# Kernel optimization log

Measured on AMD Instinct MI355X. Metric: run time of the kernel, lower is better.

Reference implementation:

```python
import jax, jax.numpy as jnp
import numpy as np

B, T, LQ, LC = 8, 256, 20, 10
DIM, H = 128, 8
VDIM, WDIM, CDIM = 1024, 300, 50
WORDS, CHARS = 10000, 100


def _build_edges(T, B):
    """Replicates build_graph_edges(hops=2) + build_semantic_edges + build_query_edges,
    then expand_edge_index_for_batch with num_nodes = T + 1.  Static numpy (jit-safe)."""
    N = T + 1
    es = []
    for h in (1, 2):  # temporal edges, 2 hops (indices replicate original code exactly)
        i = np.arange(T - h)
        es += [np.stack([i, i + h]), np.stack([i + h, i])]
    i = np.arange(T)  # query<->segment edges inside build_graph_edges
    z = np.zeros(T, dtype=np.int64)
    es += [np.stack([z, i + 1]), np.stack([i + 1, z])]
    temporal = np.concatenate(es, axis=1)
    a, b = np.triu_indices(T, k=1)  # torch.combinations(arange(T), r=2)
    sem = np.concatenate([np.stack([a, b]), np.stack([b, a])], axis=1)
    qe = np.stack([np.concatenate([[0], np.arange(1, T + 1)]),
                   np.concatenate([np.arange(1, T + 1), [0]])])
    off = (np.arange(B, dtype=np.int64) * N)[None, :, None]
    expand = lambda e: (e[:, None, :].astype(np.int64) + off).reshape(2, -1)
    return np.concatenate([expand(temporal), expand(sem), expand(qe)], axis=1)


def setup_inputs() -> dict:
    key = jax.random.key(0)
    ks = jax.random.split(key, 16)
    w = lambda k, shape: jax.random.normal(k, shape, jnp.float32) * 0.02
    return {
        "word_ids": jax.random.randint(ks[0], (B, LQ), 0, WORDS),
        "char_ids": jax.random.randint(ks[1], (B, LQ, LC), 0, CHARS),
        "video_features": jax.random.normal(ks[2], (B, T, VDIM), jnp.float32),
        "v_mask": jnp.ones((B, T), jnp.float32),
        "q_mask": jnp.ones((B, LQ), jnp.float32),
        "word_emb": w(ks[3], (WORDS, WDIM)),
        "char_emb": w(ks[4], (CHARS, CDIM)),
        "W_embed": w(ks[5], (WDIM + CDIM, DIM)), "b_embed": jnp.zeros((DIM,), jnp.float32),
        "W_vproj": w(ks[6], (VDIM, DIM)), "b_vproj": jnp.zeros((DIM,), jnp.float32),
        "W_enc": w(ks[7], (DIM, DIM)), "b_enc": jnp.zeros((DIM,), jnp.float32),
        "Wq": w(ks[8], (DIM, DIM)), "bq": jnp.zeros((DIM,), jnp.float32),
        "Wk": w(ks[9], (DIM, DIM)), "bk": jnp.zeros((DIM,), jnp.float32),
        "Wv": w(ks[10], (DIM, DIM)), "bv": jnp.zeros((DIM,), jnp.float32),
        "Wskip": w(ks[11], (DIM, DIM)), "bskip": jnp.zeros((DIM,), jnp.float32),
        "W_start": w(ks[12], (DIM, 1)), "b_start": jnp.zeros((1,), jnp.float32),
        "W_end": w(ks[13], (DIM, 1)), "b_end": jnp.zeros((1,), jnp.float32),
    }


def reference(word_ids, char_ids, video_features, v_mask, q_mask,
              word_emb, char_emb, W_embed, b_embed, W_vproj, b_vproj,
              W_enc, b_enc, Wq, bq, Wk, bk, Wv, bv, Wskip, bskip,
              W_start, b_start, W_end, b_end):
    enc = lambda x, m: jax.nn.relu(x @ W_enc + b_enc) * m[..., None]  # shared feature encoder (stand-in)
    # video branch
    vfeat = enc(video_features @ W_vproj + b_vproj, v_mask)            # [B, T, DIM]
    # query branch: word + char embeddings -> dim, encode, mean-pool
    qemb = jnp.concatenate([word_emb[word_ids], char_emb[char_ids].mean(axis=2)], axis=-1)
    qfeat = enc(qemb @ W_embed + b_embed, q_mask).mean(axis=1)         # [B, DIM]
    nodes = jnp.concatenate([qfeat[:, None, :], vfeat], axis=1)        # [B, N, DIM], N = T+1
    Bn, N, _ = nodes.shape
    Nn = Bn * N
    xf = nodes.reshape(Nn, DIM)
    edges = jnp.asarray(_build_edges(N - 1, Bn))                       # [2, E] static
    src, dst = edges[0], edges[1]                                      # PyG: messages x_j=src -> target i=dst
    hd = DIM // H
    q = (xf @ Wq + bq).reshape(Nn, H, hd)
    k = (xf @ Wk + bk).reshape(Nn, H, hd)
    v = (xf @ Wv + bv).reshape(Nn, H, hd)
    # TransformerConv: per-edge attention logits, segment-softmax over incoming edges
    logits = (q[dst] * k[src]).sum(-1) / float(np.sqrt(hd))            # [E, H]
    mx = jax.ops.segment_max(logits, dst, num_segments=Nn)
    ex = jnp.exp(logits - mx[dst])
    den = jax.ops.segment_sum(ex, dst, num_segments=Nn)
    alpha = ex / (den[dst] + 1e-16)
    agg = jax.ops.segment_sum(alpha[:, :, None] * v[src], dst, num_segments=Nn)  # [Nn, H, hd]
    out = agg.reshape(Nn, DIM) + xf @ Wskip + bskip                    # root_weight skip connection
    out = out.reshape(Bn, N, DIM)
    start_logits = (out[:, 1:] @ W_start + b_start)[..., 0]            # [B, T]
    end_logits = (out[:, 1:] @ W_end + b_end)[..., 0]                  # [B, T]
    return start_logits, end_logits
```

## Files before the change

### kernel.cpp

```cpp
#include <hip/hip_runtime.h>
#include <hip/hip_bf16.h>
#include <math.h>

#define B_ 8
#define T_ 256
#define LQ_ 20
#define LC_ 10
#define DIM_ 128
#define N_ 257
#define NN_ (B_*N_)

#define FMA4(a, s, ww) { (a).x += (s)*(ww).x; (a).y += (s)*(ww).y; (a).z += (s)*(ww).z; (a).w += (s)*(ww).w; }

__global__ __launch_bounds__(512) void kNODE(
    const float* __restrict__ video, const float* __restrict__ Wv,
    const float* __restrict__ bvp,
    const float* __restrict__ We, const float* __restrict__ be,
    const float* __restrict__ vmask,
    const int* __restrict__ word_ids, const int* __restrict__ char_ids,
    const float* __restrict__ word_emb, const float* __restrict__ char_emb,
    const float* __restrict__ W_embed, const float* __restrict__ b_embed,
    const float* __restrict__ q_mask,
    const float* __restrict__ Wq, const float* __restrict__ bq,
    const float* __restrict__ Wk, const float* __restrict__ bk,
    const float* __restrict__ Wvv, const float* __restrict__ bval,
    const float* __restrict__ Ws, const float* __restrict__ bs,
    float* __restrict__ q, float* __restrict__ k,
    float* __restrict__ v, float* __restrict__ sk,
    float* __restrict__ eq)
{
  __shared__ __align__(16) float smem_f[19008];
  float4* ps4 = reinterpret_cast<float4*>(smem_f);
  float* hl = smem_f + 16896;
  float* xe = smem_f + 17952;
  const int blk = blockIdx.x, tid = threadIdx.x;
  const float* Wm[4] = {Wq, Wk, Wvv, Ws};
  const float* bm[4] = {bq, bk, bval, bs};
  float* om[4] = {q, k, v, sk};

  if (blk < 256) {
    const int r0 = blk * 8;
    {
      const float4* src = reinterpret_cast<const float4*>(video + (size_t)r0 * 1024);
      #pragma unroll
      for (int i = 0; i < 4; ++i) {
        const int idx4 = tid + i * 512;
        const int r = idx4 >> 8, f = idx4 & 255;
        *reinterpret_cast<float4*>(&smem_f[r * 1028 + f * 4]) = src[r * 256 + f];
      }
    }
    __syncthreads();
    const int c4 = tid & 31, ks = tid >> 5;
    float4 acc[8];
    #pragma unroll
    for (int r = 0; r < 8; ++r) acc[r] = float4{0.f, 0.f, 0.f, 0.f};
    {
      const float4* W4 = reinterpret_cast<const float4*>(Wv) + c4;
      for (int kc = 0; kc < 16; ++kc) {
        const int k0 = ks * 64 + kc * 4;
        const float4 w0 = W4[(size_t)(k0 + 0) * 32];
        const float4 w1 = W4[(size_t)(k0 + 1) * 32];
        const float4 w2 = W4[(size_t)(k0 + 2) * 32];
        const float4 w3 = W4[(size_t)(k0 + 3) * 32];
        #pragma unroll
        for (int r = 0; r < 8; ++r) {
          const float4 rv = *reinterpret_cast<const float4*>(&smem_f[r * 1028 + k0]);
          FMA4(acc[r], rv.x, w0); FMA4(acc[r], rv.y, w1);
          FMA4(acc[r], rv.z, w2); FMA4(acc[r], rv.w, w3);
        }
      }
    }
    __syncthreads();
    #pragma unroll
    for (int r = 0; r < 8; ++r) ps4[(ks * 8 + r) * 33 + c4] = acc[r];
    __syncthreads();
    if (tid < 256) {
      const int r = tid >> 5, c = tid & 31;
      float4 s = reinterpret_cast<const float4*>(bvp)[c];
      #pragma unroll
      for (int ke = 0; ke < 16; ++ke) {
        const float4 p = ps4[(ke * 8 + r) * 33 + c];
        s.x += p.x; s.y += p.y; s.z += p.z; s.w += p.w;
      }
      *reinterpret_cast<float4*>(&hl[r * 132 + c * 4]) = s;
    }
    __syncthreads();
    #pragma unroll
    for (int r = 0; r < 8; ++r) acc[r] = float4{0.f, 0.f, 0.f, 0.f};
    {
      const float4* We4 = reinterpret_cast<const float4*>(We) + c4;
      #pragma unroll
      for (int kc = 0; kc < 2; ++kc) {
        const int k0 = ks * 8 + kc * 4;
        const float4 w0 = We4[(size_t)(k0 + 0) * 32];
        const float4 w1 = We4[(size_t)(k0 + 1) * 32];
        const float4 w2 = We4[(size_t)(k0 + 2) * 32];
        const float4 w3 = We4[(size_t)(k0 + 3) * 32];
        #pragma unroll
        for (int r = 0; r < 8; ++r) {
          const float4 rv = *reinterpret_cast<const float4*>(&hl[r * 132 + k0]);
          FMA4(acc[r], rv.x, w0); FMA4(acc[r], rv.y, w1);
          FMA4(acc[r], rv.z, w2); FMA4(acc[r], rv.w, w3);
        }
      }
    }
    #pragma unroll
    for (int r = 0; r < 8; ++r) ps4[(ks * 8 + r) * 33 + c4] = acc[r];
    __syncthreads();
    if (tid < 256) {
      const int r = tid >> 5, c = tid & 31;
      float4 s = reinterpret_cast<const float4*>(be)[c];
      #pragma unroll
      for (int ke = 0; ke < 16; ++ke) {
        const float4 p = ps4[(ke * 8 + r) * 33 + c];
        s.x += p.x; s.y += p.y; s.z += p.z; s.w += p.w;
      }
      const float mk = vmask[r0 + r];
      s.x = fmaxf(s.x, 0.f) * mk; s.y = fmaxf(s.y, 0.f) * mk;
      s.z = fmaxf(s.z, 0.f) * mk; s.w = fmaxf(s.w, 0.f) * mk;
      *reinterpret_cast<float4*>(&xe[r * 132 + c * 4]) = s;
    }
    __syncthreads();
    const int m = ks >> 2, keP = ks & 3;
    #pragma unroll
    for (int r = 0; r < 8; ++r) acc[r] = float4{0.f, 0.f, 0.f, 0.f};
    {
      const float4* Wp4 = reinterpret_cast<const float4*>(Wm[m]) + c4;
      #pragma unroll
      for (int kc = 0; kc < 8; ++kc) {
        const int k0 = keP * 32 + kc * 4;
        const float4 w0 = Wp4[(size_t)(k0 + 0) * 32];
        const float4 w1 = Wp4[(size_t)(k0 + 1) * 32];
        const float4 w2 = Wp4[(size_t)(k0 + 2) * 32];
        const float4 w3 = Wp4[(size_t)(k0 + 3) * 32];
        #pragma unroll
        for (int r = 0; r < 8; ++r) {
          const float4 rv = *reinterpret_cast<const float4*>(&xe[r * 132 + k0]);
          FMA4(acc[r], rv.x, w0); FMA4(acc[r], rv.y, w1);
          FMA4(acc[r], rv.z, w2); FMA4(acc[r], rv.w, w3);
        }
      }
    }
    #pragma unroll
    for (int r = 0; r < 8; ++r) ps4[(ks * 8 + r) * 33 + c4] = acc[r];
    __syncthreads();
    #pragma unroll
    for (int it = 0; it < 2; ++it) {
      const int id = tid + it * 512;
      const int mm = id >> 8, r = (id >> 5) & 7, c = id & 31;
      float4 s = reinterpret_cast<const float4*>(bm[mm])[c];
      #pragma unroll
      for (int ke = 0; ke < 4; ++ke) {
        const float4 p = ps4[((mm * 4 + ke) * 8 + r) * 33 + c];
        s.x += p.x; s.y += p.y; s.z += p.z; s.w += p.w;
      }
      const int vr = r0 + r;
      const int node = (vr >> 8) * 257 + 1 + (vr & 255);
      *reinterpret_cast<float4*>(om[mm] + (size_t)node * 128 + 4 * c) = s;
    }
  } else {
    const int qi = blk - 256;
    const int b = qi / 20, lq = qi - b * 20;
    float* emb = smem_f;
    float* ps  = emb + 352;
    float* hq  = emb + 608;
    float* pe  = emb + 736;
    const int wid = word_ids[b * LQ_ + lq];
    for (int m2 = tid; m2 < 300; m2 += 512) emb[m2] = word_emb[(size_t)wid * 300 + m2];
    if (tid < 50) {
      float s = 0.f;
      #pragma unroll
      for (int l = 0; l < 10; ++l) {
        const int cid = char_ids[(b * LQ_ + lq) * 10 + l];
        s += char_emb[cid * 50 + tid];
      }
      emb[300 + tid] = s * 0.1f;
    }
    __syncthreads();
    const int j = tid & 127, half = tid >> 7;
    if (tid < 256) {
      float a = 0.f;
      const float* Wcol = W_embed + (size_t)(half * 175) * 128 + j;
      const float* eh = emb + half * 175;
      #pragma unroll 5
      for (int m2 = 0; m2 < 175; ++m2) a += eh[m2] * Wcol[(size_t)m2 * 128];
      ps[half * 128 + j] = a;
    }
    __syncthreads();
    if (tid < 128) hq[tid] = ps[tid] + ps[128 + tid] + b_embed[tid];
    __syncthreads();
    if (tid < 256) {
      float e = 0.f;
      #pragma unroll 8
      for (int kk = 0; kk < 64; ++kk)
        e += hq[half * 64 + kk] * We[(half * 64 + kk) * 128 + j];
      pe[half * 128 + j] = e;
    }
    __syncthreads();
    if (tid < 128) {
      float ev = pe[tid] + pe[128 + tid] + be[tid];
      ev = fmaxf(ev, 0.f) * q_mask[b * LQ_ + lq];
      eq[(size_t)qi * 128 + tid] = ev;
    }
  }
}

__device__ __forceinline__ float cntf(int dnode, int s) {
  if (dnode == 256) return (s == 0 ? 1.f : 0.f) + (s == 255 ? 1.f : 0.f);
  float c = (s != dnode) ? 1.f : 0.f;
  if (s == 0) c += 1.f;
  if (s == dnode - 1) c += 2.f;
  if (s == dnode + 1 && dnode <= 254) c += 1.f;
  if (s == dnode - 2 && dnode >= 2) c += 1.f;
  if (s == dnode + 2 && dnode <= 253) c += 1.f;
  return c;
}

__global__ __launch_bounds__(256) void kATTN(
    const float* __restrict__ q, const float* __restrict__ k,
    const float* __restrict__ v, const float* __restrict__ eq,
    const float* __restrict__ Wk, const float* __restrict__ bk,
    const float* __restrict__ Wvv, const float* __restrict__ bval,
    float* __restrict__ npart, float* __restrict__ dpart)
{
  __shared__ float Kl[32][128];
  __shared__ float Vl[32][128];
  __shared__ float m0[128];
  const int d0 = blockIdx.x * 32;
  const int y  = blockIdx.y;
  const int b  = blockIdx.z;
  const int tid = threadIdx.x;
  const int base = b * 257;
  const int s0 = y * 32;
  {
    const float4* ksrc = reinterpret_cast<const float4*>(k + (size_t)(base + s0) * 128);
    const float4* vsrc = reinterpret_cast<const float4*>(v + (size_t)(base + s0) * 128);
    float4* kd = reinterpret_cast<float4*>(Kl);
    float4* vd = reinterpret_cast<float4*>(Vl);
    #pragma unroll
    for (int i = 0; i < 4; ++i) {
      kd[tid + i * 256] = ksrc[tid + i * 256];
      vd[tid + i * 256] = vsrc[tid + i * 256];
    }
  }
  if (y == 0 && tid < 128) {
    float s = 0.f;
    #pragma unroll 4
    for (int lq = 0; lq < LQ_; ++lq) s += eq[((size_t)b * LQ_ + lq) * 128 + tid];
    m0[tid] = s * (1.f / LQ_);
  }
  const int dd = tid >> 3, h = tid & 7;
  const int dnode = d0 + dd + 1;
  const float* qrow = q + (size_t)(base + dnode) * 128 + h * 16;
  const float4 qq0 = *(const float4*)(qrow + 0);
  const float4 qq1 = *(const float4*)(qrow + 4);
  const float4 qq2 = *(const float4*)(qrow + 8);
  const float4 qq3 = *(const float4*)(qrow + 12);
  __syncthreads();
  if (y == 0) {
    const int j = tid & 127, half = tid >> 7;
    const float* W = half ? Wvv : Wk;
    float acc = half ? bval[j] : bk[j];
    #pragma unroll 8
    for (int kk = 0; kk < 128; ++kk) acc += m0[kk] * W[kk * 128 + j];
    if (half) Vl[0][j] = acc; else Kl[0][j] = acc;
  }
  __syncthreads();

  float den = 0.f;
  float4 o0 = {0,0,0,0}, o1 = {0,0,0,0}, o2 = {0,0,0,0}, o3 = {0,0,0,0};
  #pragma unroll 2
  for (int s = 0; s < 32; ++s) {
    const float* krow = &Kl[s][h * 16];
    const float4 k0 = *(const float4*)(krow + 0);
    const float4 k1 = *(const float4*)(krow + 4);
    const float4 k2 = *(const float4*)(krow + 8);
    const float4 k3 = *(const float4*)(krow + 12);
    float dt = qq0.x*k0.x + qq0.y*k0.y + qq0.z*k0.z + qq0.w*k0.w
             + qq1.x*k1.x + qq1.y*k1.y + qq1.z*k1.z + qq1.w*k1.w
             + qq2.x*k2.x + qq2.y*k2.y + qq2.z*k2.z + qq2.w*k2.w
             + qq3.x*k3.x + qq3.y*k3.y + qq3.z*k3.z + qq3.w*k3.w;
    const float c = cntf(dnode, s0 + s);
    const float pw = c * __expf(dt * 0.25f);
    den += pw;
    const float* vrow = &Vl[s][h * 16];
    const float4 v0 = *(const float4*)(vrow + 0);
    const float4 v1 = *(const float4*)(vrow + 4);
    const float4 v2 = *(const float4*)(vrow + 8);
    const float4 v3 = *(const float4*)(vrow + 12);
    o0.x += pw*v0.x; o0.y += pw*v0.y; o0.z += pw*v0.z; o0.w += pw*v0.w;
    o1.x += pw*v1.x; o1.y += pw*v1.y; o1.z += pw*v1.z; o1.w += pw*v1.w;
    o2.x += pw*v2.x; o2.y += pw*v2.y; o2.z += pw*v2.z; o2.w += pw*v2.w;
    o3.x += pw*v3.x; o3.y += pw*v3.y; o3.z += pw*v3.z; o3.w += pw*v3.w;
  }
  const size_t pb = ((size_t)y * 8 + b) * 256 + d0;
  float* np = npart + (pb + dd) * 128 + h * 16;
  *reinterpret_cast<float4*>(np + 0)  = o0;
  *reinterpret_cast<float4*>(np + 4)  = o1;
  *reinterpret_cast<float4*>(np + 8)  = o2;
  *reinterpret_cast<float4*>(np + 12) = o3;
  dpart[(pb + dd) * 8 + h] = den;
}

__global__ __launch_bounds__(256) void kRED(
    const float* __restrict__ npart, const float* __restrict__ dpart,
    const float* __restrict__ sk,
    const float* __restrict__ W_start, const float* __restrict__ b_start,
    const float* __restrict__ W_end, const float* __restrict__ b_end,
    float* __restrict__ out)
{
  __shared__ float red[16][2][2];
  const int d0 = blockIdx.x * 16;
  const int b = blockIdx.y;
  const int tid = threadIdx.x;
  const int base = b * 257;
  const int jB = tid & 127, shB = tid >> 7;
  const int hB = jB >> 4;
  const float wst = W_start[jB], wen = W_end[jB];
  #pragma unroll
  for (int dd8 = 0; dd8 < 8; ++dd8) {
    const int dd = shB * 8 + dd8;
    const int dst = d0 + dd;
    float num = 0.f, den = 0.f;
    #pragma unroll
    for (int y = 0; y < 8; ++y) {
      const size_t pb = ((size_t)y * 8 + b) * 256 + dst;
      num += npart[pb * 128 + jB];
      den += dpart[pb * 8 + hB];
    }
    const float o = num / (den + 1e-16f) + sk[(size_t)(base + dst + 1) * 128 + jB];
    float psum = o * wst, pesum = o * wen;
    #pragma unroll
    for (int off = 1; off < 64; off <<= 1) {
      psum += __shfl_xor(psum, off);
      pesum += __shfl_xor(pesum, off);
    }
    if ((tid & 63) == 0) { red[dd][jB >> 6][0] = psum; red[dd][jB >> 6][1] = pesum; }
  }
  __syncthreads();
  if (tid < 16) {
    out[b * 256 + d0 + tid]        = red[tid][0][0] + red[tid][1][0] + b_start[0];
    out[2048 + b * 256 + d0 + tid] = red[tid][0][1] + red[tid][1][1] + b_end[0];
  }
}

extern "C" void kernel_launch(void* const* d_in, const int* in_sizes, int n_in,
                              void* d_out, int out_size, void* d_ws, size_t ws_size,
                              hipStream_t stream) {
  const int*   word_ids = (const int*)d_in[0];
  const int*   char_ids = (const int*)d_in[1];
  const float* video    = (const float*)d_in[2];
  const float* v_mask   = (const float*)d_in[3];
  const float* q_mask   = (const float*)d_in[4];
  const float* word_emb = (const float*)d_in[5];
  const float* char_emb = (const float*)d_in[6];
  const float* W_embed  = (const float*)d_in[7];
  const float* b_embed  = (const float*)d_in[8];
  const float* W_vproj  = (const float*)d_in[9];
  const float* b_vproj  = (const float*)d_in[10];
  const float* W_enc    = (const float*)d_in[11];
  const float* b_enc    = (const float*)d_in[12];
  const float* Wq       = (const float*)d_in[13];
  const float* bq       = (const float*)d_in[14];
  const float* Wk       = (const float*)d_in[15];
  const float* bk       = (const float*)d_in[16];
  const float* Wv       = (const float*)d_in[17];
  const float* bv       = (const float*)d_in[18];
  const float* Wskip    = (const float*)d_in[19];
  const float* bskip    = (const float*)d_in[20];
  const float* W_start  = (const float*)d_in[21];
  const float* b_start  = (const float*)d_in[22];
  const float* W_end    = (const float*)d_in[23];
  const float* b_end    = (const float*)d_in[24];

  float* q     = (float*)d_ws;
  float* k     = q  + NN_ * DIM_;
  float* v     = k  + NN_ * DIM_;
  float* sk    = v  + NN_ * DIM_;
  float* eq    = sk + NN_ * DIM_;
  float* npart = eq + 160 * 128;
  float* dpart = npart + (size_t)8 * 8 * 256 * 128;

  hipLaunchKernelGGL(kNODE, dim3(416), dim3(512), 0, stream,
    video, W_vproj, b_vproj, W_enc, b_enc, v_mask,
    word_ids, char_ids, word_emb, char_emb, W_embed, b_embed, q_mask,
    Wq, bq, Wk, bk, Wv, bv, Wskip, bskip, q, k, v, sk, eq);
  hipLaunchKernelGGL(kATTN, dim3(8, 8, 8), dim3(256), 0, stream,
    q, k, v, eq, Wk, bk, Wv, bv, npart, dpart);
  hipLaunchKernelGGL(kRED, dim3(16, 8), dim3(256), 0, stream,
    npart, dpart, sk, W_start, b_start, W_end, b_end, (float*)d_out);
}
```

Measured before the change: 60.48 us.

## Move video projection GEMM onto bf16 MFMA with split-precision hi/lo operands

The 2048x1024x128 video projection now runs in its own kernel using bf16 MFMA instructions instead of fp32 FMA loops. Each fp32 operand is split into high and low bf16 parts, and three MFMA products are summed to keep accuracy close to fp32. A pre-kernel converts W_vproj to transposed hi/lo bf16 every call and also computes the query embeddings. The K dimension is split across two blocks whose partial sums are added in the follow-on kernel. The goal is to replace the slow fp32 FMA GEMM with matrix-core throughput, at the cost of two extra launches, extra global round trips for the partials and converted weights, and small precision differences.

```diff
diff --git a/kernel.cpp b/kernel.cpp
--- a/kernel.cpp
+++ b/kernel.cpp
@@ -12,22 +12,169 @@
 
 #define FMA4(a, s, ww) { (a).x += (s)*(ww).x; (a).y += (s)*(ww).y; (a).z += (s)*(ww).z; (a).w += (s)*(ww).w; }
 
-__global__ __launch_bounds__(512) void kNODE(
-    const float* __restrict__ video, const float* __restrict__ Wv,
-    const float* __restrict__ bvp,
-    const float* __restrict__ We, const float* __restrict__ be,
-    const float* __restrict__ vmask,
+typedef __attribute__((ext_vector_type(8))) short bf16x8;
+typedef __attribute__((ext_vector_type(4))) float f32x4;
+
+__device__ __forceinline__ unsigned short f2bf(float f) {
+  unsigned u = __float_as_uint(f);
+  unsigned r = u + 0x7FFFu + ((u >> 16) & 1u);
+  return (unsigned short)(r >> 16);
+}
+__device__ __forceinline__ float bf2f(unsigned short h) {
+  return __uint_as_float(((unsigned)h) << 16);
+}
+
+__global__ __launch_bounds__(256) void kPRE(
     const int* __restrict__ word_ids, const int* __restrict__ char_ids,
     const float* __restrict__ word_emb, const float* __restrict__ char_emb,
     const float* __restrict__ W_embed, const float* __restrict__ b_embed,
+    const float* __restrict__ We, const float* __restrict__ be,
     const float* __restrict__ q_mask,
+    const float* __restrict__ Wv,
+    float* __restrict__ eq,
+    unsigned short* __restrict__ WvTh, unsigned short* __restrict__ WvTl)
+{
+  __shared__ __align__(16) float smem[2112];
+  const int blk = blockIdx.x, tid = threadIdx.x;
+  if (blk < 160) {
+    const int qi = blk;
+    const int b = qi / 20, lq = qi - b * 20;
+    float* emb = smem;
+    float* ps  = emb + 352;
+    float* hq  = emb + 608;
+    float* pe  = emb + 736;
+    const int wid = word_ids[b * LQ_ + lq];
+    for (int m2 = tid; m2 < 300; m2 += 256) emb[m2] = word_emb[(size_t)wid * 300 + m2];
+    if (tid < 50) {
+      float s = 0.f;
+      #pragma unroll
+      for (int l = 0; l < 10; ++l) {
+        const int cid = char_ids[(b * LQ_ + lq) * 10 + l];
+        s += char_emb[cid * 50 + tid];
+      }
+      emb[300 + tid] = s * 0.1f;
+    }
+    __syncthreads();
+    const int j = tid & 127, half = tid >> 7;
+    {
+      float a = 0.f;
+      const float* Wcol = W_embed + (size_t)(half * 175) * 128 + j;
+      const float* eh = emb + half * 175;
+      #pragma unroll 5
+      for (int m2 = 0; m2 < 175; ++m2) a += eh[m2] * Wcol[(size_t)m2 * 128];
+      ps[half * 128 + j] = a;
+    }
+    __syncthreads();
+    if (tid < 128) hq[tid] = ps[tid] + ps[128 + tid] + b_embed[tid];
+    __syncthreads();
+    {
+      float e = 0.f;
+      #pragma unroll 8
+      for (int kk = 0; kk < 64; ++kk)
+        e += hq[half * 64 + kk] * We[(half * 64 + kk) * 128 + j];
+      pe[half * 128 + j] = e;
+    }
+    __syncthreads();
+    if (tid < 128) {
+      float ev = pe[tid] + pe[128 + tid] + be[tid];
+      ev = fmaxf(ev, 0.f) * q_mask[b * LQ_ + lq];
+      eq[(size_t)qi * 128 + tid] = ev;
+    }
+  } else {
+    const int k0 = (blk - 160) * 16;
+    const float4* src = reinterpret_cast<const float4*>(Wv + (size_t)k0 * 128);
+    #pragma unroll
+    for (int i = 0; i < 2; ++i) {
+      const int idx4 = tid + i * 256;
+      const int r = idx4 >> 5, f = idx4 & 31;
+      *reinterpret_cast<float4*>(&smem[r * 132 + f * 4]) = src[r * 32 + f];
+    }
+    __syncthreads();
+    const int col = tid & 127, kg = tid >> 7;
+    bf16x8 vh, vl;
+    #pragma unroll
+    for (int j = 0; j < 8; ++j) {
+      const int kk = kg * 8 + j;
+      const float xv = smem[kk * 132 + col];
+      const unsigned short hi = f2bf(xv);
+      const unsigned short lo = f2bf(xv - bf2f(hi));
+      vh[j] = (short)hi; vl[j] = (short)lo;
+    }
+    *reinterpret_cast<bf16x8*>(WvTh + (size_t)col * 1024 + k0 + kg * 8) = vh;
+    *reinterpret_cast<bf16x8*>(WvTl + (size_t)col * 1024 + k0 + kg * 8) = vl;
+  }
+}
+
+__global__ __launch_bounds__(512) void kVID(
+    const float* __restrict__ video,
+    const unsigned short* __restrict__ WvTh,
+    const unsigned short* __restrict__ WvTl,
+    float* __restrict__ h2)
+{
+  __shared__ unsigned short Ah[16 * 512];
+  __shared__ unsigned short Al[16 * 512];
+  const int blk = blockIdx.x, tid = threadIdx.x;
+  const int rt = blk >> 1, kh = blk & 1;
+  const int r0 = rt * 16;
+  #pragma unroll
+  for (int i = 0; i < 2; ++i) {
+    const int g = tid * 2 + i;
+    const int row = g >> 6, gk = g & 63;
+    const float* src = video + (size_t)(r0 + row) * 1024 + kh * 512 + gk * 8;
+    const float4 x0 = *reinterpret_cast<const float4*>(src);
+    const float4 x1 = *reinterpret_cast<const float4*>(src + 4);
+    const float xs[8] = {x0.x, x0.y, x0.z, x0.w, x1.x, x1.y, x1.z, x1.w};
+    bf16x8 vh, vl;
+    #pragma unroll
+    for (int j = 0; j < 8; ++j) {
+      const unsigned short hi = f2bf(xs[j]);
+      const unsigned short lo = f2bf(xs[j] - bf2f(hi));
+      vh[j] = (short)hi; vl[j] = (short)lo;
+    }
+    int byteoff = row * 1024 + gk * 16;
+    byteoff ^= ((row & 7) << 4);
+    *reinterpret_cast<bf16x8*>(reinterpret_cast<char*>(Ah) + byteoff) = vh;
+    *reinterpret_cast<bf16x8*>(reinterpret_cast<char*>(Al) + byteoff) = vl;
+  }
+  __syncthreads();
+  const int wv = tid >> 6, lane = tid & 63;
+  const int col16 = lane & 15, kg8 = lane >> 4;
+  const int c0 = wv * 16;
+  const unsigned short* pBh = WvTh + (size_t)(c0 + col16) * 1024 + kh * 512;
+  const unsigned short* pBl = WvTl + (size_t)(c0 + col16) * 1024 + kh * 512;
+  const int arow = lane & 15;
+  const int abase = arow * 1024;
+  f32x4 acc = {0.f, 0.f, 0.f, 0.f};
+  #pragma unroll 4
+  for (int t = 0; t < 16; ++t) {
+    const int kb = t * 32 + kg8 * 8;
+    const int aoff = (abase + kb * 2) ^ ((arow & 7) << 4);
+    const bf16x8 ah = *reinterpret_cast<const bf16x8*>(reinterpret_cast<const char*>(Ah) + aoff);
+    const bf16x8 al = *reinterpret_cast<const bf16x8*>(reinterpret_cast<const char*>(Al) + aoff);
+    const bf16x8 bh = *reinterpret_cast<const bf16x8*>(pBh + kb);
+    const bf16x8 bl = *reinterpret_cast<const bf16x8*>(pBl + kb);
+    acc = __builtin_amdgcn_mfma_f32_16x16x32_bf16(ah, bh, acc, 0, 0, 0);
+    acc = __builtin_amdgcn_mfma_f32_16x16x32_bf16(ah, bl, acc, 0, 0, 0);
+    acc = __builtin_amdgcn_mfma_f32_16x16x32_bf16(al, bh, acc, 0, 0, 0);
+  }
+  const int ocol = c0 + col16;
+  const int orow = (lane >> 4) * 4;
+  float* hdst = h2 + (size_t)kh * 2048 * 128;
+  #pragma unroll
+  for (int i2 = 0; i2 < 4; ++i2)
+    hdst[(size_t)(r0 + orow + i2) * 128 + ocol] = acc[i2];
+}
+
+__global__ __launch_bounds__(512) void kMAIN(
+    const float* __restrict__ h2, const float* __restrict__ bvp,
+    const float* __restrict__ We, const float* __restrict__ be,
+    const float* __restrict__ vmask,
     const float* __restrict__ Wq, const float* __restrict__ bq,
     const float* __restrict__ Wk, const float* __restrict__ bk,
     const float* __restrict__ Wvv, const float* __restrict__ bval,
     const float* __restrict__ Ws, const float* __restrict__ bs,
     float* __restrict__ q, float* __restrict__ k,
-    float* __restrict__ v, float* __restrict__ sk,
-    float* __restrict__ eq)
+    float* __restrict__ v, float* __restrict__ sk)
 {
   __shared__ __align__(16) float smem_f[19008];
   float4* ps4 = reinterpret_cast<float4*>(smem_f);
@@ -37,171 +184,91 @@
   const float* Wm[4] = {Wq, Wk, Wvv, Ws};
   const float* bm[4] = {bq, bk, bval, bs};
   float* om[4] = {q, k, v, sk};
-
-  if (blk < 256) {
-    const int r0 = blk * 8;
-    {
-      const float4* src = reinterpret_cast<const float4*>(video + (size_t)r0 * 1024);
+  const int r0 = blk * 8;
+  if (tid < 256) {
+    const int r = tid >> 5, c = tid & 31;
+    const float4 p0 = *reinterpret_cast<const float4*>(h2 + (size_t)(r0 + r) * 128 + c * 4);
+    const float4 p1 = *reinterpret_cast<const float4*>(h2 + (size_t)(2048 + r0 + r) * 128 + c * 4);
+    float4 s = reinterpret_cast<const float4*>(bvp)[c];
+    s.x += p0.x + p1.x; s.y += p0.y + p1.y;
+    s.z += p0.z + p1.z; s.w += p0.w + p1.w;
+    *reinterpret_cast<float4*>(&hl[r * 132 + c * 4]) = s;
+  }
+  __syncthreads();
+  const int c4 = tid & 31, ks = tid >> 5;
+  float4 acc[8];
+  #pragma unroll
+  for (int r = 0; r < 8; ++r) acc[r] = float4{0.f, 0.f, 0.f, 0.f};
+  {
+    const float4* We4 = reinterpret_cast<const float4*>(We) + c4;
+    #pragma unroll
+    for (int kc = 0; kc < 2; ++kc) {
+      const int k0 = ks * 8 + kc * 4;
+      const float4 w0 = We4[(size_t)(k0 + 0) * 32];
+      const float4 w1 = We4[(size_t)(k0 + 1) * 32];
+      const float4 w2 = We4[(size_t)(k0 + 2) * 32];
+      const float4 w3 = We4[(size_t)(k0 + 3) * 32];
       #pragma unroll
-      for (int i = 0; i < 4; ++i) {
-        const int idx4 = tid + i * 512;
-        const int r = idx4 >> 8, f = idx4 & 255;
-        *reinterpret_cast<float4*>(&smem_f[r * 1028 + f * 4]) = src[r * 256 + f];
+      for (int r = 0; r < 8; ++r) {
+        const float4 rv = *reinterpret_cast<const float4*>(&hl[r * 132 + k0]);
+        FMA4(acc[r], rv.x, w0); FMA4(acc[r], rv.y, w1);
+        FMA4(acc[r], rv.z, w2); FMA4(acc[r], rv.w, w3);
       }
     }
-    __syncthreads();
-    const int c4 = tid & 31, ks = tid >> 5;
-    float4 acc[8];
-    #pragma unroll
-    for (int r = 0; r < 8; ++r) acc[r] = float4{0.f, 0.f, 0.f, 0.f};
-    {
-      const float4* W4 = reinterpret_cast<const float4*>(Wv) + c4;
-      for (int kc = 0; kc < 16; ++kc) {
-        const int k0 = ks * 64 + kc * 4;
-        const float4 w0 = W4[(size_t)(k0 + 0) * 32];
-        const float4 w1 = W4[(size_t)(k0 + 1) * 32];
-        const float4 w2 = W4[(size_t)(k0 + 2) * 32];
-        const float4 w3 = W4[(size_t)(k0 + 3) * 32];
-        #pragma unroll
-        for (int r = 0; r < 8; ++r) {
-          const float4 rv = *reinterpret_cast<const float4*>(&smem_f[r * 1028 + k0]);
-          FMA4(acc[r], rv.x, w0); FMA4(acc[r], rv.y, w1);
-          FMA4(acc[r], rv.z, w2); FMA4(acc[r], rv.w, w3);
-        }
+  }
+  #pragma unroll
+  for (int r = 0; r < 8; ++r) ps4[(ks * 8 + r) * 33 + c4] = acc[r];
+  __syncthreads();
+  if (tid < 256) {
+    const int r = tid >> 5, c = tid & 31;
+    float4 s = reinterpret_cast<const float4*>(be)[c];
+    #pragma unroll
+    for (int ke = 0; ke < 16; ++ke) {
+      const float4 p = ps4[(ke * 8 + r) * 33 + c];
+      s.x += p.x; s.y += p.y; s.z += p.z; s.w += p.w;
+    }
+    const float mk = vmask[r0 + r];
+    s.x = fmaxf(s.x, 0.f) * mk; s.y = fmaxf(s.y, 0.f) * mk;
+    s.z = fmaxf(s.z, 0.f) * mk; s.w = fmaxf(s.w, 0.f) * mk;
+    *reinterpret_cast<float4*>(&xe[r * 132 + c * 4]) = s;
+  }
+  __syncthreads();
+  const int m = ks >> 2, keP = ks & 3;
+  #pragma unroll
+  for (int r = 0; r < 8; ++r) acc[r] = float4{0.f, 0.f, 0.f, 0.f};
+  {
+    const float4* Wp4 = reinterpret_cast<const float4*>(Wm[m]) + c4;
+    #pragma unroll
+    for (int kc = 0; kc < 8; ++kc) {
+      const int k0 = keP * 32 + kc * 4;
+      const float4 w0 = Wp4[(size_t)(k0 + 0) * 32];
+      const float4 w1 = Wp4[(size_t)(k0 + 1) * 32];
+      const float4 w2 = Wp4[(size_t)(k0 + 2) * 32];
+      const float4 w3 = Wp4[(size_t)(k0 + 3) * 32];
+      #pragma unroll
+      for (int r = 0; r < 8; ++r) {
+        const float4 rv = *reinterpret_cast<const float4*>(&xe[r * 132 + k0]);
+        FMA4(acc[r], rv.x, w0); FMA4(acc[r], rv.y, w1);
+        FMA4(acc[r], rv.z, w2); FMA4(acc[r], rv.w, w3);
       }
     }
-    __syncthreads();
-    #pragma unroll
-    for (int r = 0; r < 8; ++r) ps4[(ks * 8 + r) * 33 + c4] = acc[r];
-    __syncthreads();
-    if (tid < 256) {
-      const int r = tid >> 5, c = tid & 31;
-      float4 s = reinterpret_cast<const float4*>(bvp)[c];
-      #pragma unroll
-      for (int ke = 0; ke < 16; ++ke) {
-        const float4 p = ps4[(ke * 8 + r) * 33 + c];
-        s.x += p.x; s.y += p.y; s.z += p.z; s.w += p.w;
-      }
-      *reinterpret_cast<float4*>(&hl[r * 132 + c * 4]) = s;
-    }
-    __syncthreads();
-    #pragma unroll
-    for (int r = 0; r < 8; ++r) acc[r] = float4{0.f, 0.f, 0.f, 0.f};
-    {
-      const float4* We4 = reinterpret_cast<const float4*>(We) + c4;
-      #pragma unroll
-      for (int kc = 0; kc < 2; ++kc) {
-        const int k0 = ks * 8 + kc * 4;
-        const float4 w0 = We4[(size_t)(k0 + 0) * 32];
-        const float4 w1 = We4[(size_t)(k0 + 1) * 32];
-        const float4 w2 = We4[(size_t)(k0 + 2) * 32];
-        const float4 w3 = We4[(size_t)(k0 + 3) * 32];
-        #pragma unroll
-        for (int r = 0; r < 8; ++r) {
-          const float4 rv = *reinterpret_cast<const float4*>(&hl[r * 132 + k0]);
-          FMA4(acc[r], rv.x, w0); FMA4(acc[r], rv.y, w1);
-          FMA4(acc[r], rv.z, w2); FMA4(acc[r], rv.w, w3);
-        }
-      }
-    }
-    #pragma unroll
-    for (int r = 0; r < 8; ++r) ps4[(ks * 8 + r) * 33 + c4] = acc[r];
-    __syncthreads();
-    if (tid < 256) {
-      const int r = tid >> 5, c = tid & 31;
-      float4 s = reinterpret_cast<const float4*>(be)[c];
-      #pragma unroll
-      for (int ke = 0; ke < 16; ++ke) {
-        const float4 p = ps4[(ke * 8 + r) * 33 + c];
-        s.x += p.x; s.y += p.y; s.z += p.z; s.w += p.w;
-      }
-      const float mk = vmask[r0 + r];
-      s.x = fmaxf(s.x, 0.f) * mk; s.y = fmaxf(s.y, 0.f) * mk;
-      s.z = fmaxf(s.z, 0.f) * mk; s.w = fmaxf(s.w, 0.f) * mk;
-      *reinterpret_cast<float4*>(&xe[r * 132 + c * 4]) = s;
-    }
-    __syncthreads();
-    const int m = ks >> 2, keP = ks & 3;
-    #pragma unroll
-    for (int r = 0; r < 8; ++r) acc[r] = float4{0.f, 0.f, 0.f, 0.f};
-    {
-      const float4* Wp4 = reinterpret_cast<const float4*>(Wm[m]) + c4;
-      #pragma unroll
-      for (int kc = 0; kc < 8; ++kc) {
-        const int k0 = keP * 32 + kc * 4;
-        const float4 w0 = Wp4[(size_t)(k0 + 0) * 32];
-        const float4 w1 = Wp4[(size_t)(k0 + 1) * 32];
-        const float4 w2 = Wp4[(size_t)(k0 + 2) * 32];
-        const float4 w3 = Wp4[(size_t)(k0 + 3) * 32];
-        #pragma unroll
-        for (int r = 0; r < 8; ++r) {
-          const float4 rv = *reinterpret_cast<const float4*>(&xe[r * 132 + k0]);
-          FMA4(acc[r], rv.x, w0); FMA4(acc[r], rv.y, w1);
-          FMA4(acc[r], rv.z, w2); FMA4(acc[r], rv.w, w3);
-        }
-      }
-    }
-    #pragma unroll
-    for (int r = 0; r < 8; ++r) ps4[(ks * 8 + r) * 33 + c4] = acc[r];
-    __syncthreads();
-    #pragma unroll
-    for (int it = 0; it < 2; ++it) {
-      const int id = tid + it * 512;
-      const int mm = id >> 8, r = (id >> 5) & 7, c = id & 31;
-      float4 s = reinterpret_cast<const float4*>(bm[mm])[c];
-      #pragma unroll
-      for (int ke = 0; ke < 4; ++ke) {
-        const float4 p = ps4[((mm * 4 + ke) * 8 + r) * 33 + c];
-        s.x += p.x; s.y += p.y; s.z += p.z; s.w += p.w;
-      }
-      const int vr = r0 + r;
-      const int node = (vr >> 8) * 257 + 1 + (vr & 255);
-      *reinterpret_cast<float4*>(om[mm] + (size_t)node * 128 + 4 * c) = s;
-    }
-  } else {
-    const int qi = blk - 256;
-    const int b = qi / 20, lq = qi - b * 20;
-    float* emb = smem_f;
-    float* ps  = emb + 352;
-    float* hq  = emb + 608;
-    float* pe  = emb + 736;
-    const int wid = word_ids[b * LQ_ + lq];
-    for (int m2 = tid; m2 < 300; m2 += 512) emb[m2] = word_emb[(size_t)wid * 300 + m2];
-    if (tid < 50) {
-      float s = 0.f;
-      #pragma unroll
-      for (int l = 0; l < 10; ++l) {
-        const int cid = char_ids[(b * LQ_ + lq) * 10 + l];
-        s += char_emb[cid * 50 + tid];
-      }
-      emb[300 + tid] = s * 0.1f;
-    }
-    __syncthreads();
-    const int j = tid & 127, half = tid >> 7;
-    if (tid < 256) {
-      float a = 0.f;
-      const float* Wcol = W_embed + (size_t)(half * 175) * 128 + j;
-      const float* eh = emb + half * 175;
-      #pragma unroll 5
-      for (int m2 = 0; m2 < 175; ++m2) a += eh[m2] * Wcol[(size_t)m2 * 128];
-      ps[half * 128 + j] = a;
-    }
-    __syncthreads();
-    if (tid < 128) hq[tid] = ps[tid] + ps[128 + tid] + b_embed[tid];
-    __syncthreads();
-    if (tid < 256) {
-      float e = 0.f;
-      #pragma unroll 8
-      for (int kk = 0; kk < 64; ++kk)
-        e += hq[half * 64 + kk] * We[(half * 64 + kk) * 128 + j];
-      pe[half * 128 + j] = e;
-    }
-    __syncthreads();
-    if (tid < 128) {
-      float ev = pe[tid] + pe[128 + tid] + be[tid];
-      ev = fmaxf(ev, 0.f) * q_mask[b * LQ_ + lq];
-      eq[(size_t)qi * 128 + tid] = ev;
-    }
+  }
+  #pragma unroll
+  for (int r = 0; r < 8; ++r) ps4[(ks * 8 + r) * 33 + c4] = acc[r];
+  __syncthreads();
+  #pragma unroll
+  for (int it = 0; it < 2; ++it) {
+    const int id = tid + it * 512;
+    const int mm = id >> 8, r = (id >> 5) & 7, c = id & 31;
+    float4 s = reinterpret_cast<const float4*>(bm[mm])[c];
+    #pragma unroll
+    for (int ke = 0; ke < 4; ++ke) {
+      const float4 p = ps4[((mm * 4 + ke) * 8 + r) * 33 + c];
+      s.x += p.x; s.y += p.y; s.z += p.z; s.w += p.w;
+    }
+    const int vr = r0 + r;
+    const int node = (vr >> 8) * 257 + 1 + (vr & 255);
+    *reinterpret_cast<float4*>(om[mm] + (size_t)node * 128 + 4 * c) = s;
   }
 }
 
@@ -380,11 +447,18 @@
   float* eq    = sk + NN_ * DIM_;
   float* npart = eq + 160 * 128;
   float* dpart = npart + (size_t)8 * 8 * 256 * 128;
-
-  hipLaunchKernelGGL(kNODE, dim3(416), dim3(512), 0, stream,
-    video, W_vproj, b_vproj, W_enc, b_enc, v_mask,
-    word_ids, char_ids, word_emb, char_emb, W_embed, b_embed, q_mask,
-    Wq, bq, Wk, bk, Wv, bv, Wskip, bskip, q, k, v, sk, eq);
+  float* h2    = dpart + 16384;
+  unsigned short* WvTh = (unsigned short*)(h2 + (size_t)2 * 2048 * 128);
+  unsigned short* WvTl = WvTh + 128 * 1024;
+
+  hipLaunchKernelGGL(kPRE, dim3(224), dim3(256), 0, stream,
+    word_ids, char_ids, word_emb, char_emb, W_embed, b_embed,
+    W_enc, b_enc, q_mask, W_vproj, eq, WvTh, WvTl);
+  hipLaunchKernelGGL(kVID, dim3(256), dim3(512), 0, stream,
+    video, WvTh, WvTl, h2);
+  hipLaunchKernelGGL(kMAIN, dim3(256), dim3(512), 0, stream,
+    h2, b_vproj, W_enc, b_enc, v_mask,
+    Wq, bq, Wk, bk, Wv, bv, Wskip, bskip, q, k, v, sk);
   hipLaunchKernelGGL(kATTN, dim3(8, 8, 8), dim3(256), 0, stream,
     q, k, v, eq, Wk, bk, Wv, bv, npart, dpart);
   hipLaunchKernelGGL(kRED, dim3(16, 8), dim3(256), 0, stream,
```

After: 65.49 us. 8.3% more time.

## Project V onto start/end heads before attention to shrink partial outputs

Applied to the files above, without the earlier changes.

Because the start and end heads are linear, each V row is pre-multiplied by the W_start and W_end head slices inside the attention kernel. Each query then accumulates two scalars per head instead of a 16-wide vector. This cuts the partial-numerator buffer from 128 floats per node per split to 2 per head, and removes most of the reduction kernel's global reads. The cost is an extra small shared-memory projection and sync per block, plus a change in floating-point summation order.

```diff
diff --git a/kernel.cpp b/kernel.cpp
--- a/kernel.cpp
+++ b/kernel.cpp
@@ -221,11 +221,15 @@
     const float* __restrict__ v, const float* __restrict__ eq,
     const float* __restrict__ Wk, const float* __restrict__ bk,
     const float* __restrict__ Wvv, const float* __restrict__ bval,
-    float* __restrict__ npart, float* __restrict__ dpart)
+    const float* __restrict__ W_start, const float* __restrict__ W_end,
+    float* __restrict__ nst_p, float* __restrict__ nen_p,
+    float* __restrict__ den_p)
 {
   __shared__ float Kl[32][128];
   __shared__ float Vl[32][128];
   __shared__ float m0[128];
+  __shared__ float vstl[32][8];
+  __shared__ float venl[32][8];
   const int d0 = blockIdx.x * 32;
   const int y  = blockIdx.y;
   const int b  = blockIdx.z;
@@ -266,10 +270,20 @@
     if (half) Vl[0][j] = acc; else Kl[0][j] = acc;
   }
   __syncthreads();
-
-  float den = 0.f;
-  float4 o0 = {0,0,0,0}, o1 = {0,0,0,0}, o2 = {0,0,0,0}, o3 = {0,0,0,0};
-  #pragma unroll 2
+  {
+    const int sv = tid >> 3, hv = tid & 7;
+    const float* vr = &Vl[sv][hv * 16];
+    const float* wst = W_start + hv * 16;
+    const float* wen = W_end + hv * 16;
+    float a = 0.f, e = 0.f;
+    #pragma unroll
+    for (int i = 0; i < 16; ++i) { a += vr[i] * wst[i]; e += vr[i] * wen[i]; }
+    vstl[sv][hv] = a; venl[sv][hv] = e;
+  }
+  __syncthreads();
+
+  float den = 0.f, nst = 0.f, nen = 0.f;
+  #pragma unroll 4
   for (int s = 0; s < 32; ++s) {
     const float* krow = &Kl[s][h * 16];
     const float4 k0 = *(const float4*)(krow + 0);
@@ -283,52 +297,52 @@
     const float c = cntf(dnode, s0 + s);
     const float pw = c * __expf(dt * 0.25f);
     den += pw;
-    const float* vrow = &Vl[s][h * 16];
-    const float4 v0 = *(const float4*)(vrow + 0);
-    const float4 v1 = *(const float4*)(vrow + 4);
-    const float4 v2 = *(const float4*)(vrow + 8);
-    const float4 v3 = *(const float4*)(vrow + 12);
-    o0.x += pw*v0.x; o0.y += pw*v0.y; o0.z += pw*v0.z; o0.w += pw*v0.w;
-    o1.x += pw*v1.x; o1.y += pw*v1.y; o1.z += pw*v1.z; o1.w += pw*v1.w;
-    o2.x += pw*v2.x; o2.y += pw*v2.y; o2.z += pw*v2.z; o2.w += pw*v2.w;
-    o3.x += pw*v3.x; o3.y += pw*v3.y; o3.z += pw*v3.z; o3.w += pw*v3.w;
-  }
-  const size_t pb = ((size_t)y * 8 + b) * 256 + d0;
-  float* np = npart + (pb + dd) * 128 + h * 16;
-  *reinterpret_cast<float4*>(np + 0)  = o0;
-  *reinterpret_cast<float4*>(np + 4)  = o1;
-  *reinterpret_cast<float4*>(np + 8)  = o2;
-  *reinterpret_cast<float4*>(np + 12) = o3;
-  dpart[(pb + dd) * 8 + h] = den;
+    nst += pw * vstl[s][h];
+    nen += pw * venl[s][h];
+  }
+  const size_t pb = (((size_t)y * 8 + b) * 256 + d0 + dd) * 8 + h;
+  nst_p[pb] = nst; nen_p[pb] = nen; den_p[pb] = den;
 }
 
 __global__ __launch_bounds__(256) void kRED(
-    const float* __restrict__ npart, const float* __restrict__ dpart,
-    const float* __restrict__ sk,
+    const float* __restrict__ nst_p, const float* __restrict__ nen_p,
+    const float* __restrict__ den_p, const float* __restrict__ sk,
     const float* __restrict__ W_start, const float* __restrict__ b_start,
     const float* __restrict__ W_end, const float* __restrict__ b_end,
     float* __restrict__ out)
 {
+  __shared__ float attst[16], atten[16];
   __shared__ float red[16][2][2];
   const int d0 = blockIdx.x * 16;
   const int b = blockIdx.y;
   const int tid = threadIdx.x;
   const int base = b * 257;
+  if (tid < 128) {
+    const int dd = tid >> 3, h = tid & 7;
+    const int dst = d0 + dd;
+    float den = 0.f, nst = 0.f, nen = 0.f;
+    #pragma unroll
+    for (int y = 0; y < 8; ++y) {
+      const size_t pb = (((size_t)y * 8 + b) * 256 + dst) * 8 + h;
+      nst += nst_p[pb]; nen += nen_p[pb]; den += den_p[pb];
+    }
+    float rst = nst / (den + 1e-16f);
+    float ren = nen / (den + 1e-16f);
+    #pragma unroll
+    for (int off = 1; off < 8; off <<= 1) {
+      rst += __shfl_xor(rst, off);
+      ren += __shfl_xor(ren, off);
+    }
+    if (h == 0) { attst[dd] = rst; atten[dd] = ren; }
+  }
+  __syncthreads();
   const int jB = tid & 127, shB = tid >> 7;
-  const int hB = jB >> 4;
   const float wst = W_start[jB], wen = W_end[jB];
   #pragma unroll
   for (int dd8 = 0; dd8 < 8; ++dd8) {
     const int dd = shB * 8 + dd8;
     const int dst = d0 + dd;
-    float num = 0.f, den = 0.f;
-    #pragma unroll
-    for (int y = 0; y < 8; ++y) {
-      const size_t pb = ((size_t)y * 8 + b) * 256 + dst;
-      num += npart[pb * 128 + jB];
-      den += dpart[pb * 8 + hB];
-    }
-    const float o = num / (den + 1e-16f) + sk[(size_t)(base + dst + 1) * 128 + jB];
+    const float o = sk[(size_t)(base + dst + 1) * 128 + jB];
     float psum = o * wst, pesum = o * wen;
     #pragma unroll
     for (int off = 1; off < 64; off <<= 1) {
@@ -339,8 +353,8 @@
   }
   __syncthreads();
   if (tid < 16) {
-    out[b * 256 + d0 + tid]        = red[tid][0][0] + red[tid][1][0] + b_start[0];
-    out[2048 + b * 256 + d0 + tid] = red[tid][0][1] + red[tid][1][1] + b_end[0];
+    out[b * 256 + d0 + tid]        = red[tid][0][0] + red[tid][1][0] + attst[tid] + b_start[0];
+    out[2048 + b * 256 + d0 + tid] = red[tid][0][1] + red[tid][1][1] + atten[tid] + b_end[0];
   }
 }
 
@@ -378,15 +392,16 @@
   float* v     = k  + NN_ * DIM_;
   float* sk    = v  + NN_ * DIM_;
   float* eq    = sk + NN_ * DIM_;
-  float* npart = eq + 160 * 128;
-  float* dpart = npart + (size_t)8 * 8 * 256 * 128;
+  float* nst_p = eq + 160 * 128;
+  float* nen_p = nst_p + 131072;
+  float* den_p = nen_p + 131072;
 
   hipLaunchKernelGGL(kNODE, dim3(416), dim3(512), 0, stream,
     video, W_vproj, b_vproj, W_enc, b_enc, v_mask,
     word_ids, char_ids, word_emb, char_emb, W_embed, b_embed, q_mask,
     Wq, bq, Wk, bk, Wv, bv, Wskip, bskip, q, k, v, sk, eq);
   hipLaunchKernelGGL(kATTN, dim3(8, 8, 8), dim3(256), 0, stream,
-    q, k, v, eq, Wk, bk, Wv, bv, npart, dpart);
+    q, k, v, eq, Wk, bk, Wv, bv, W_start, W_end, nst_p, nen_p, den_p);
   hipLaunchKernelGGL(kRED, dim3(16, 8), dim3(256), 0, stream,
-    npart, dpart, sk, W_start, b_start, W_end, b_end, (float*)d_out);
+    nst_p, nen_p, den_p, sk, W_start, b_start, W_end, b_end, (float*)d_out);
 }
```

After: 58.52 us, median of 2. 3.2% less time.
